# Performance work log

Measured on AMD Instinct MI355X. Metric: run time of the kernel, lower is better.

The kernel has to match this reference:

```python
import jax, jax.numpy as jnp
import numpy as np

T, B, H = 1024, 16, 1024
S = 2048


def setup_inputs() -> dict:
    key = jax.random.key(0)
    k1, k2, k3, k4 = jax.random.split(key, 4)
    output = jax.random.normal(k1, (T, B, H), dtype=jnp.float32)
    memory = jax.random.normal(k2, (S, B, H), dtype=jnp.float32)
    attn_mask = jnp.zeros((B, T, S), dtype=jnp.bool_)  # True = masked
    # linear_out: Linear(2H -> H); torch weight layout [out, in]
    W = jax.random.normal(k3, (H, 2 * H), dtype=jnp.float32) * (1.0 / np.sqrt(2 * H))
    b = jax.random.normal(k4, (H,), dtype=jnp.float32) * 0.01
    return {"output": output, "memory": memory, "attn_mask": attn_mask, "W": W, "b": b}


def reference(output, memory, attn_mask, W, b):
    # scores: (B, T, S) = output^T @ memory (unscaled dot product)
    attn = jnp.einsum('tbh,sbh->bts', output, memory)
    attn = jnp.where(attn_mask, -jnp.inf, attn)
    attn = jax.nn.softmax(attn, axis=2)
    # context: (T, B, H)
    context = jnp.einsum('bts,sbh->tbh', attn, memory)
    combined = jnp.concatenate([context, output], axis=2)  # (T, B, 2H)
    out = jnp.tanh(jnp.einsum('tbd,hd->tbh', combined, W) + b)
    return (out, attn)
```

## Files before the change

### kernel.cpp

```cpp
#include <hip/hip_runtime.h>
#include <hip/hip_bf16.h>
#include <math.h>

#define Tn 1024
#define Bn 16
#define Hn 1024
#define Sn 2048

typedef __attribute__((ext_vector_type(8))) short bf16x8;
typedef __attribute__((ext_vector_type(8))) unsigned short u16x8;
typedef __attribute__((ext_vector_type(4))) float f32x4;

__device__ __forceinline__ unsigned short f2bf(float x) {
  unsigned u = __float_as_uint(x);
  u += 0x7fffu + ((u >> 16) & 1u);
  return (unsigned short)(u >> 16);
}
__device__ __forceinline__ float bf2f(unsigned short h) {
  return __uint_as_float(((unsigned)h) << 16);
}

__device__ __forceinline__ void gload16(const void* g, void* l) {
  __builtin_amdgcn_global_load_lds((const __attribute__((address_space(1))) void*)g,
                                   (__attribute__((address_space(3))) void*)l, 16, 0, 0);
}


__global__ __launch_bounds__(256) void k_split_plane(const float* __restrict__ src,
                                                     unsigned short* __restrict__ hiP,
                                                     unsigned short* __restrict__ loP,
                                                     int rows) {
  const int i = blockIdx.x * 256 + threadIdx.x;
  const int h8 = i & (Hn / 8 - 1);
  const int rem = i >> 7;
  const int b = rem & (Bn - 1);
  const int r = rem >> 4;
  const float4 a = *(const float4*)(src + (size_t)i * 8);
  const float4 c = *(const float4*)(src + (size_t)i * 8 + 4);
  const float v[8] = {a.x, a.y, a.z, a.w, c.x, c.y, c.z, c.w};
  u16x8 hv, lv;
#pragma unroll
  for (int j = 0; j < 8; ++j) {
    const unsigned short h = f2bf(v[j]);
    hv[j] = h;
    lv[j] = f2bf(v[j] - bf2f(h));
  }
  const size_t dst = ((size_t)b * rows + r) * Hn + h8 * 8;
  *(u16x8*)(hiP + dst) = hv;
  *(u16x8*)(loP + dst) = lv;
}

__global__ __launch_bounds__(256) void k_cvt8(const float* __restrict__ src,
                                              unsigned short* __restrict__ dst, int n8) {
  const int i = blockIdx.x * 256 + threadIdx.x;
  if (i >= n8) return;
  const float4 a = *(const float4*)(src + (size_t)i * 8);
  const float4 c = *(const float4*)(src + (size_t)i * 8 + 4);
  u16x8 u;
  u[0] = f2bf(a.x); u[1] = f2bf(a.y); u[2] = f2bf(a.z); u[3] = f2bf(a.w);
  u[4] = f2bf(c.x); u[5] = f2bf(c.y); u[6] = f2bf(c.z); u[7] = f2bf(c.w);
  *(u16x8*)(dst + (size_t)i * 8) = u;
}

__global__ __launch_bounds__(256) void k_trH(const unsigned short* __restrict__ memH,
                                             unsigned short* __restrict__ memT) {
  __shared__ unsigned short L[64 * 72];
  const int t = threadIdx.x;
  const int h0 = blockIdx.x * 64, s0 = blockIdx.y * 64, b = blockIdx.z;
#pragma unroll
  for (int p = 0; p < 2; ++p) {
    const int fid = p * 256 + t;
    const int s_l = fid >> 3;
    const int c = fid & 7;
    const u16x8 v = *(const u16x8*)(memH + ((size_t)b * Sn + s0 + s_l) * Hn + h0 + c * 8);
#pragma unroll
    for (int e = 0; e < 8; ++e) L[(c * 8 + e) * 72 + s_l] = v[e];
  }
  __syncthreads();
#pragma unroll
  for (int p = 0; p < 2; ++p) {
    const int cid = p * 256 + t;
    const int h_l = cid >> 3;
    const int c = cid & 7;
    const u16x8 vv = *(const u16x8*)&L[h_l * 72 + c * 8];
    *(u16x8*)(memT + ((size_t)b * Hn + h0 + h_l) * Sn + s0 + c * 8) = vv;
  }
}


__device__ __forceinline__ void stage128x32(const unsigned short* __restrict__ g, size_t ldr,
                                            unsigned short* __restrict__ lds, int tid) {
  const int wv = tid >> 6;
  const int row = tid >> 2;
  const size_t coff = (size_t)(tid & 3) * 8;
#pragma unroll
  for (int q = 0; q < 2; ++q)
    gload16(g + (size_t)(q * 64 + row) * ldr + coff, lds + q * 2048 + wv * 512);
}

__device__ __forceinline__ void stage128x64(const unsigned short* __restrict__ g, size_t ldr,
                                            unsigned short* __restrict__ lds, int tid) {
  const int wv = tid >> 6;
  const int row = tid >> 3;
  const size_t coff = (size_t)(tid & 7) * 8;
#pragma unroll
  for (int q = 0; q < 4; ++q)
    gload16(g + (size_t)(q * 32 + row) * ldr + coff, lds + q * 2048 + wv * 512);
}


__global__ __launch_bounds__(256, 2) void k_scores(const unsigned short* __restrict__ oH,
                                                   const unsigned short* __restrict__ oL,
                                                   const unsigned short* __restrict__ mH,
                                                   const unsigned short* __restrict__ mL,
                                                   float* __restrict__ attn) {
  __shared__ unsigned short AsH[2][128 * 32], AsL[2][128 * 32];
  __shared__ unsigned short BsH[2][128 * 32], BsL[2][128 * 32];
  const int tid = threadIdx.x, lane = tid & 63, wv = tid >> 6;
  const int wm = (wv >> 1) * 64, wn = (wv & 1) * 64;
  const int bs = blockIdx.x * 128, bt = blockIdx.y * 128, b = blockIdx.z;
  const f32x4 fz = {0.f, 0.f, 0.f, 0.f};
  f32x4 acc[4][4];
#pragma unroll
  for (int i = 0; i < 4; ++i)
#pragma unroll
    for (int j = 0; j < 4; ++j) acc[i][j] = fz;

  const unsigned short* AgH = oH + ((size_t)b * Tn + bt) * Hn;
  const unsigned short* AgL = oL + ((size_t)b * Tn + bt) * Hn;
  const unsigned short* BgH = mH + ((size_t)b * Sn + bs) * Hn;
  const unsigned short* BgL = mL + ((size_t)b * Sn + bs) * Hn;
  const int r16 = lane & 15, kh = (lane >> 4) * 8;
  const int NK = Hn / 32;

  stage128x32(AgH, Hn, AsH[0], tid);
  stage128x32(AgL, Hn, AsL[0], tid);
  stage128x32(BgH, Hn, BsH[0], tid);
  stage128x32(BgL, Hn, BsL[0], tid);
  __syncthreads();

#pragma unroll 2
  for (int t = 0; t < NK; ++t) {
    const int cur = t & 1;
    if (t + 1 < NK) {
      const int k0 = (t + 1) * 32;
      stage128x32(AgH + k0, Hn, AsH[cur ^ 1], tid);
      stage128x32(AgL + k0, Hn, AsL[cur ^ 1], tid);
      stage128x32(BgH + k0, Hn, BsH[cur ^ 1], tid);
      stage128x32(BgL + k0, Hn, BsL[cur ^ 1], tid);
    }
    const unsigned short* AH = AsH[cur];
    const unsigned short* AL = AsL[cur];
    const unsigned short* BH = BsH[cur];
    const unsigned short* BL = BsL[cur];
    bf16x8 ah[4], al[4];
#pragma unroll
    for (int i = 0; i < 4; ++i) {
      ah[i] = *(const bf16x8*)&AH[(wm + i * 16 + r16) * 32 + kh];
      al[i] = *(const bf16x8*)&AL[(wm + i * 16 + r16) * 32 + kh];
    }
#pragma unroll
    for (int j = 0; j < 4; ++j) {
      const bf16x8 bh = *(const bf16x8*)&BH[(wn + j * 16 + r16) * 32 + kh];
      const bf16x8 bl = *(const bf16x8*)&BL[(wn + j * 16 + r16) * 32 + kh];
#pragma unroll
      for (int i = 0; i < 4; ++i) {
        acc[i][j] = __builtin_amdgcn_mfma_f32_16x16x32_bf16(ah[i], bh, acc[i][j], 0, 0, 0);
        acc[i][j] = __builtin_amdgcn_mfma_f32_16x16x32_bf16(ah[i], bl, acc[i][j], 0, 0, 0);
        acc[i][j] = __builtin_amdgcn_mfma_f32_16x16x32_bf16(al[i], bh, acc[i][j], 0, 0, 0);
      }
    }
    __syncthreads();
  }
  const int rq = (lane >> 4) * 4;
  float* obase = attn + (size_t)b * Tn * Sn;
#pragma unroll
  for (int i = 0; i < 4; ++i)
#pragma unroll
    for (int q = 0; q < 4; ++q) {
      const int t = bt + wm + i * 16 + rq + q;
#pragma unroll
      for (int j = 0; j < 4; ++j) {
        const int s = bs + wn + j * 16 + r16;
        obase[(size_t)t * Sn + s] = acc[i][j][q];
      }
    }
}


__global__ __launch_bounds__(256) void k_softmax(float* __restrict__ attn,
                                                 const unsigned char* __restrict__ mask,
                                                 unsigned short* __restrict__ attnbf) {
  const int row = blockIdx.x;
  float* p = attn + (size_t)row * Sn;
  const unsigned char* mrow = mask + (size_t)row * Sn;
  const int tid = threadIdx.x;
  const int lane = tid & 63;
  const int wv = tid >> 6;
  const float4 a = *(const float4*)(p + tid * 8);
  const float4 c = *(const float4*)(p + tid * 8 + 4);
  const unsigned long long mv = *(const unsigned long long*)(mrow + tid * 8);
  float x[8] = {a.x, a.y, a.z, a.w, c.x, c.y, c.z, c.w};
#pragma unroll
  for (int j = 0; j < 8; ++j)
    if ((mv >> (8 * j)) & 0xffull) x[j] = -INFINITY;
  float mx = x[0];
#pragma unroll
  for (int j = 1; j < 8; ++j) mx = fmaxf(mx, x[j]);
#pragma unroll
  for (int off = 32; off; off >>= 1) mx = fmaxf(mx, __shfl_xor(mx, off, 64));
  __shared__ float redmax[4], redsum[4];
  if (lane == 0) redmax[wv] = mx;
  __syncthreads();
  mx = fmaxf(fmaxf(redmax[0], redmax[1]), fmaxf(redmax[2], redmax[3]));
  float e[8];
  float s = 0.f;
#pragma unroll
  for (int j = 0; j < 8; ++j) {
    e[j] = __expf(x[j] - mx);
    s += e[j];
  }
#pragma unroll
  for (int off = 32; off; off >>= 1) s += __shfl_xor(s, off, 64);
  if (lane == 0) redsum[wv] = s;
  __syncthreads();
  s = redsum[0] + redsum[1] + redsum[2] + redsum[3];
  const float inv = 1.0f / s;
  float o[8];
#pragma unroll
  for (int j = 0; j < 8; ++j) o[j] = e[j] * inv;
  float4 o0 = {o[0], o[1], o[2], o[3]};
  float4 o1 = {o[4], o[5], o[6], o[7]};
  *(float4*)(p + tid * 8) = o0;
  *(float4*)(p + tid * 8 + 4) = o1;
  u16x8 ub;
#pragma unroll
  for (int j = 0; j < 8; ++j) ub[j] = f2bf(o[j]);
  *(u16x8*)(attnbf + (size_t)row * Sn + tid * 8) = ub;
}


__device__ __forceinline__ void mfma64(const unsigned short* __restrict__ A,
                                       const unsigned short* __restrict__ B,
                                       int wm, int wn, int lane, f32x4 (&acc)[4][4]) {
  const int r16 = lane & 15;
  const int kh = (lane >> 4) * 8;
#pragma unroll
  for (int ks = 0; ks < 2; ++ks) {
    bf16x8 a[4], bb[4];
#pragma unroll
    for (int i = 0; i < 4; ++i) a[i] = *(const bf16x8*)&A[(wm + i * 16 + r16) * 64 + ks * 32 + kh];
#pragma unroll
    for (int j = 0; j < 4; ++j) bb[j] = *(const bf16x8*)&B[(wn + j * 16 + r16) * 64 + ks * 32 + kh];
#pragma unroll
    for (int i = 0; i < 4; ++i)
#pragma unroll
      for (int j = 0; j < 4; ++j)
        acc[i][j] = __builtin_amdgcn_mfma_f32_16x16x32_bf16(a[i], bb[j], acc[i][j], 0, 0, 0);
  }
}

__global__ __launch_bounds__(256, 2) void k_context(const unsigned short* __restrict__ attnbf,
                                                    const unsigned short* __restrict__ memT,
                                                    unsigned short* __restrict__ ctxB) {
  __shared__ unsigned short As[2][128 * 64], Bs[2][128 * 64];
  const int tid = threadIdx.x, lane = tid & 63, wv = tid >> 6;
  const int wm = (wv >> 1) * 64, wn = (wv & 1) * 64;
  const int bh = blockIdx.x * 128, bt = blockIdx.y * 128, b = blockIdx.z;
  const f32x4 fz = {0.f, 0.f, 0.f, 0.f};
  f32x4 acc[4][4];
#pragma unroll
  for (int i = 0; i < 4; ++i)
#pragma unroll
    for (int j = 0; j < 4; ++j) acc[i][j] = fz;

  const unsigned short* Ag = attnbf + ((size_t)b * Tn + bt) * Sn;
  const unsigned short* Bg = memT + ((size_t)b * Hn + bh) * Sn;
  const int NK = Sn / 64;
  stage128x64(Ag, Sn, As[0], tid);
  stage128x64(Bg, Sn, Bs[0], tid);
  __syncthreads();
#pragma unroll 2
  for (int t = 0; t < NK; ++t) {
    const int cur = t & 1;
    if (t + 1 < NK) {
      const int k0 = (t + 1) * 64;
      stage128x64(Ag + k0, Sn, As[cur ^ 1], tid);
      stage128x64(Bg + k0, Sn, Bs[cur ^ 1], tid);
    }
    mfma64(As[cur], Bs[cur], wm, wn, lane, acc);
    __syncthreads();
  }
  const int r16 = lane & 15, rq = (lane >> 4) * 4;
#pragma unroll
  for (int i = 0; i < 4; ++i)
#pragma unroll
    for (int q = 0; q < 4; ++q) {
      const int t = bt + wm + i * 16 + rq + q;
#pragma unroll
      for (int j = 0; j < 4; ++j) {
        const int h = bh + wn + j * 16 + r16;
        ctxB[((size_t)b * Tn + t) * Hn + h] = f2bf(acc[i][j][q]);
      }
    }
}

__global__ __launch_bounds__(256, 2) void k_final(const unsigned short* __restrict__ ctxB,
                                                  const unsigned short* __restrict__ outpH,
                                                  const unsigned short* __restrict__ Wbf,
                                                  const float* __restrict__ bias,
                                                  float* __restrict__ out) {
  __shared__ unsigned short As[2][128 * 64], Bs[2][128 * 64];
  const int tid = threadIdx.x, lane = tid & 63, wv = tid >> 6;
  const int wm = (wv >> 1) * 64, wn = (wv & 1) * 64;
  const int bh = blockIdx.x * 128, bm = blockIdx.y * 128;
  const f32x4 fz = {0.f, 0.f, 0.f, 0.f};
  f32x4 acc[4][4];
#pragma unroll
  for (int i = 0; i < 4; ++i)
#pragma unroll
    for (int j = 0; j < 4; ++j) acc[i][j] = fz;

  const int NK = (2 * Hn) / 64;
  auto Asrc = [&](int t) -> const unsigned short* {
    const int k0 = t * 64;
    return (k0 < Hn) ? (ctxB + (size_t)bm * Hn + k0) : (outpH + (size_t)bm * Hn + (k0 - Hn));
  };
  stage128x64(Asrc(0), Hn, As[0], tid);
  stage128x64(Wbf + (size_t)bh * (2 * Hn), 2 * Hn, Bs[0], tid);
  __syncthreads();
#pragma unroll 2
  for (int t = 0; t < NK; ++t) {
    const int cur = t & 1;
    if (t + 1 < NK) {
      stage128x64(Asrc(t + 1), Hn, As[cur ^ 1], tid);
      stage128x64(Wbf + (size_t)bh * (2 * Hn) + (t + 1) * 64, 2 * Hn, Bs[cur ^ 1], tid);
    }
    mfma64(As[cur], Bs[cur], wm, wn, lane, acc);
    __syncthreads();
  }
  const int r16 = lane & 15, rq = (lane >> 4) * 4;
  float bj[4];
#pragma unroll
  for (int j = 0; j < 4; ++j) bj[j] = bias[bh + wn + j * 16 + r16];
#pragma unroll
  for (int i = 0; i < 4; ++i)
#pragma unroll
    for (int q = 0; q < 4; ++q) {
      const int r = bm + wm + i * 16 + rq + q;
      const int b = r >> 10, t = r & (Tn - 1);
#pragma unroll
      for (int j = 0; j < 4; ++j) {
        const int h = bh + wn + j * 16 + r16;
        out[((size_t)t * Bn + b) * Hn + h] = tanhf(acc[i][j][q] + bj[j]);
      }
    }
}

extern "C" void kernel_launch(void* const* d_in, const int* in_sizes, int n_in,
                              void* d_out, int out_size, void* d_ws, size_t ws_size,
                              hipStream_t stream) {
  const float* outp = (const float*)d_in[0];
  const float* mem = (const float*)d_in[1];
  const unsigned char* mask = (const unsigned char*)d_in[2];
  const float* W = (const float*)d_in[3];
  const float* bias = (const float*)d_in[4];
  float* out = (float*)d_out;
  float* attn = out + (size_t)Tn * Bn * Hn;

  char* w = (char*)d_ws;
  unsigned short* memH  = (unsigned short*)(w);
  unsigned short* memL  = (unsigned short*)(w + ((size_t)64 << 20));
  unsigned short* outpH = (unsigned short*)(w + ((size_t)128 << 20));
  unsigned short* outpL = (unsigned short*)(w + ((size_t)160 << 20));
  unsigned short* Wbf   = (unsigned short*)(w + ((size_t)192 << 20));
  unsigned short* memT   = memL;
  unsigned short* attnbf = memH;
  unsigned short* ctxB   = outpL;

  k_split_plane<<<dim3((Tn * Bn * Hn / 8) / 256), 256, 0, stream>>>(outp, outpH, outpL, Tn);
  k_split_plane<<<dim3((Sn * Bn * Hn / 8) / 256), 256, 0, stream>>>(mem, memH, memL, Sn);
  k_cvt8<<<dim3((Hn * 2 * Hn / 8) / 256), 256, 0, stream>>>(W, Wbf, Hn * 2 * Hn / 8);

  k_scores<<<dim3(Sn / 128, Tn / 128, Bn), 256, 0, stream>>>(outpH, outpL, memH, memL, attn);
  k_trH<<<dim3(Hn / 64, Sn / 64, Bn), 256, 0, stream>>>(memH, memT);
  k_softmax<<<dim3(Bn * Tn), 256, 0, stream>>>(attn, mask, attnbf);
  k_context<<<dim3(Hn / 128, Tn / 128, Bn), 256, 0, stream>>>(attnbf, memT, ctxB);
  k_final<<<dim3(Hn / 128, (Tn * Bn) / 128), 256, 0, stream>>>(ctxB, outpH, Wbf, bias, out);
}
```

Baseline: 618.1 us.

## Enlarge GEMM tiles to 256x256 with 8 waves, swizzled LDS, finer waits

The three MFMA GEMM kernels (scores, context, final) now use 256x256 block tiles with 512 threads. Each wave computes a 128x64 sub-tile, which raises data reuse per LDS load and halves the number of blocks. LDS staging uses an XOR swizzle to avoid bank conflicts. The full __syncthreads is replaced by explicit vmcnt waits plus s_barrier and s_setprio around the MFMA bursts, to overlap global loads with compute. The costs are larger LDS use (128 KB in scores), more accumulator registers, and fewer blocks, which reduces occupancy and tail balance.

```diff
diff --git a/kernel.cpp b/kernel.cpp
--- a/kernel.cpp
+++ b/kernel.cpp
@@ -88,41 +88,43 @@
 }
 
 
-__device__ __forceinline__ void stage128x32(const unsigned short* __restrict__ g, size_t ldr,
+__device__ __forceinline__ void stage256x64(const unsigned short* __restrict__ g, size_t ldr,
                                             unsigned short* __restrict__ lds, int tid) {
-  const int wv = tid >> 6;
-  const int row = tid >> 2;
-  const size_t coff = (size_t)(tid & 3) * 8;
-#pragma unroll
-  for (int q = 0; q < 2; ++q)
-    gload16(g + (size_t)(q * 64 + row) * ldr + coff, lds + q * 2048 + wv * 512);
-}
-
-__device__ __forceinline__ void stage128x64(const unsigned short* __restrict__ g, size_t ldr,
+#pragma unroll
+  for (int r = 0; r < 4; ++r) {
+    const int row = r * 64 + (tid >> 3);
+    const int cb = (tid & 7) * 16;
+    const int cs = cb ^ ((row & 4) << 3);
+    gload16((const char*)g + (size_t)row * ldr * 2 + cs, (char*)lds + r * 8192 + tid * 16);
+  }
+}
+
+__device__ __forceinline__ void stage256x32(const unsigned short* __restrict__ g, size_t ldr,
                                             unsigned short* __restrict__ lds, int tid) {
-  const int wv = tid >> 6;
-  const int row = tid >> 3;
-  const size_t coff = (size_t)(tid & 7) * 8;
-#pragma unroll
-  for (int q = 0; q < 4; ++q)
-    gload16(g + (size_t)(q * 32 + row) * ldr + coff, lds + q * 2048 + wv * 512);
-}
-
-
-__global__ __launch_bounds__(256, 2) void k_scores(const unsigned short* __restrict__ oH,
+#pragma unroll
+  for (int r = 0; r < 2; ++r) {
+    const int row = r * 128 + (tid >> 2);
+    const int cb = (tid & 3) * 16;
+    const int cs = cb ^ ((row & 8) << 2);
+    gload16((const char*)g + (size_t)row * ldr * 2 + cs, (char*)lds + r * 8192 + tid * 16);
+  }
+}
+
+
+__global__ __launch_bounds__(512, 2) void k_scores(const unsigned short* __restrict__ oH,
                                                    const unsigned short* __restrict__ oL,
                                                    const unsigned short* __restrict__ mH,
                                                    const unsigned short* __restrict__ mL,
                                                    float* __restrict__ attn) {
-  __shared__ unsigned short AsH[2][128 * 32], AsL[2][128 * 32];
-  __shared__ unsigned short BsH[2][128 * 32], BsL[2][128 * 32];
+  __shared__ unsigned short AsH[2][256 * 32], AsL[2][256 * 32];
+  __shared__ unsigned short BsH[2][256 * 32], BsL[2][256 * 32];
   const int tid = threadIdx.x, lane = tid & 63, wv = tid >> 6;
-  const int wm = (wv >> 1) * 64, wn = (wv & 1) * 64;
-  const int bs = blockIdx.x * 128, bt = blockIdx.y * 128, b = blockIdx.z;
+  const int wr = wv >> 2, wc = wv & 3;
+  const int bs = blockIdx.x * 256, bt = blockIdx.y * 256, b = blockIdx.z;
   const f32x4 fz = {0.f, 0.f, 0.f, 0.f};
-  f32x4 acc[4][4];
-#pragma unroll
-  for (int i = 0; i < 4; ++i)
+  f32x4 acc[8][4];
+#pragma unroll
+  for (int i = 0; i < 8; ++i)
 #pragma unroll
     for (int j = 0; j < 4; ++j) acc[i][j] = fz;
 
@@ -130,61 +132,83 @@
   const unsigned short* AgL = oL + ((size_t)b * Tn + bt) * Hn;
   const unsigned short* BgH = mH + ((size_t)b * Sn + bs) * Hn;
   const unsigned short* BgL = mL + ((size_t)b * Sn + bs) * Hn;
-  const int r16 = lane & 15, kh = (lane >> 4) * 8;
+  const int r16 = lane & 15, khB = (lane >> 4) * 16;
   const int NK = Hn / 32;
 
-  stage128x32(AgH, Hn, AsH[0], tid);
-  stage128x32(AgL, Hn, AsL[0], tid);
-  stage128x32(BgH, Hn, BsH[0], tid);
-  stage128x32(BgL, Hn, BsL[0], tid);
-  __syncthreads();
-
-#pragma unroll 2
+  stage256x32(AgH, Hn, AsH[0], tid);
+  stage256x32(AgL, Hn, AsL[0], tid);
+  stage256x32(BgH, Hn, BsH[0], tid);
+  stage256x32(BgL, Hn, BsL[0], tid);
+
   for (int t = 0; t < NK; ++t) {
     const int cur = t & 1;
     if (t + 1 < NK) {
       const int k0 = (t + 1) * 32;
-      stage128x32(AgH + k0, Hn, AsH[cur ^ 1], tid);
-      stage128x32(AgL + k0, Hn, AsL[cur ^ 1], tid);
-      stage128x32(BgH + k0, Hn, BsH[cur ^ 1], tid);
-      stage128x32(BgL + k0, Hn, BsL[cur ^ 1], tid);
-    }
-    const unsigned short* AH = AsH[cur];
-    const unsigned short* AL = AsL[cur];
-    const unsigned short* BH = BsH[cur];
-    const unsigned short* BL = BsL[cur];
-    bf16x8 ah[4], al[4];
-#pragma unroll
-    for (int i = 0; i < 4; ++i) {
-      ah[i] = *(const bf16x8*)&AH[(wm + i * 16 + r16) * 32 + kh];
-      al[i] = *(const bf16x8*)&AL[(wm + i * 16 + r16) * 32 + kh];
-    }
-#pragma unroll
-    for (int j = 0; j < 4; ++j) {
-      const bf16x8 bh = *(const bf16x8*)&BH[(wn + j * 16 + r16) * 32 + kh];
-      const bf16x8 bl = *(const bf16x8*)&BL[(wn + j * 16 + r16) * 32 + kh];
-#pragma unroll
-      for (int i = 0; i < 4; ++i) {
-        acc[i][j] = __builtin_amdgcn_mfma_f32_16x16x32_bf16(ah[i], bh, acc[i][j], 0, 0, 0);
-        acc[i][j] = __builtin_amdgcn_mfma_f32_16x16x32_bf16(ah[i], bl, acc[i][j], 0, 0, 0);
-        acc[i][j] = __builtin_amdgcn_mfma_f32_16x16x32_bf16(al[i], bh, acc[i][j], 0, 0, 0);
-      }
-    }
-    __syncthreads();
+      stage256x32(AgH + k0, Hn, AsH[cur ^ 1], tid);
+      stage256x32(AgL + k0, Hn, AsL[cur ^ 1], tid);
+      stage256x32(BgH + k0, Hn, BsH[cur ^ 1], tid);
+      stage256x32(BgL + k0, Hn, BsL[cur ^ 1], tid);
+      asm volatile("s_waitcnt vmcnt(8)" ::: "memory");
+    } else {
+      asm volatile("s_waitcnt vmcnt(0)" ::: "memory");
+    }
+    __builtin_amdgcn_s_barrier();
+
+    const char* ABh = (const char*)AsH[cur];
+    const char* ABl = (const char*)AsL[cur];
+    const char* BBh = (const char*)BsH[cur];
+    const char* BBl = (const char*)BsL[cur];
+    bf16x8 bh[2][2], bl[2][2];
+#pragma unroll
+    for (int nq = 0; nq < 2; ++nq)
+#pragma unroll
+      for (int fj = 0; fj < 2; ++fj) {
+        const int rb = wc * 64 + nq * 32 + fj * 16 + r16;
+        const int off = rb * 64 + (khB ^ ((rb & 8) << 2));
+        bh[nq][fj] = *(const bf16x8*)(BBh + off);
+        bl[nq][fj] = *(const bf16x8*)(BBl + off);
+      }
+#pragma unroll
+    for (int mq = 0; mq < 2; ++mq) {
+      bf16x8 ah[4], al[4];
+#pragma unroll
+      for (int fi = 0; fi < 4; ++fi) {
+        const int ra = wr * 128 + mq * 64 + fi * 16 + r16;
+        const int off = ra * 64 + (khB ^ ((ra & 8) << 2));
+        ah[fi] = *(const bf16x8*)(ABh + off);
+        al[fi] = *(const bf16x8*)(ABl + off);
+      }
+      __builtin_amdgcn_s_setprio(1);
+#pragma unroll
+      for (int nq = 0; nq < 2; ++nq)
+#pragma unroll
+        for (int fj = 0; fj < 2; ++fj)
+#pragma unroll
+          for (int fi = 0; fi < 4; ++fi) {
+            f32x4& a = acc[mq * 4 + fi][nq * 2 + fj];
+            a = __builtin_amdgcn_mfma_f32_16x16x32_bf16(ah[fi], bh[nq][fj], a, 0, 0, 0);
+            a = __builtin_amdgcn_mfma_f32_16x16x32_bf16(ah[fi], bl[nq][fj], a, 0, 0, 0);
+            a = __builtin_amdgcn_mfma_f32_16x16x32_bf16(al[fi], bh[nq][fj], a, 0, 0, 0);
+          }
+      __builtin_amdgcn_s_setprio(0);
+    }
+    __builtin_amdgcn_s_barrier();
   }
   const int rq = (lane >> 4) * 4;
   float* obase = attn + (size_t)b * Tn * Sn;
 #pragma unroll
-  for (int i = 0; i < 4; ++i)
+  for (int i = 0; i < 8; ++i) {
+    const int m_off = wr * 128 + (i >> 2) * 64 + (i & 3) * 16;
 #pragma unroll
     for (int q = 0; q < 4; ++q) {
-      const int t = bt + wm + i * 16 + rq + q;
+      const int t = bt + m_off + rq + q;
 #pragma unroll
       for (int j = 0; j < 4; ++j) {
-        const int s = bs + wn + j * 16 + r16;
+        const int s = bs + wc * 64 + (j >> 1) * 32 + (j & 1) * 16 + r16;
         obase[(size_t)t * Sn + s] = acc[i][j][q];
       }
     }
+  }
 }
 
 
@@ -240,121 +264,194 @@
 }
 
 
-__device__ __forceinline__ void mfma64(const unsigned short* __restrict__ A,
-                                       const unsigned short* __restrict__ B,
-                                       int wm, int wn, int lane, f32x4 (&acc)[4][4]) {
-  const int r16 = lane & 15;
-  const int kh = (lane >> 4) * 8;
-#pragma unroll
-  for (int ks = 0; ks < 2; ++ks) {
-    bf16x8 a[4], bb[4];
-#pragma unroll
-    for (int i = 0; i < 4; ++i) a[i] = *(const bf16x8*)&A[(wm + i * 16 + r16) * 64 + ks * 32 + kh];
-#pragma unroll
-    for (int j = 0; j < 4; ++j) bb[j] = *(const bf16x8*)&B[(wn + j * 16 + r16) * 64 + ks * 32 + kh];
-#pragma unroll
-    for (int i = 0; i < 4; ++i)
-#pragma unroll
-      for (int j = 0; j < 4; ++j)
-        acc[i][j] = __builtin_amdgcn_mfma_f32_16x16x32_bf16(a[i], bb[j], acc[i][j], 0, 0, 0);
-  }
-}
-
-__global__ __launch_bounds__(256, 2) void k_context(const unsigned short* __restrict__ attnbf,
+__global__ __launch_bounds__(512, 2) void k_context(const unsigned short* __restrict__ attnbf,
                                                     const unsigned short* __restrict__ memT,
                                                     unsigned short* __restrict__ ctxB) {
-  __shared__ unsigned short As[2][128 * 64], Bs[2][128 * 64];
+  __shared__ unsigned short As[2][256 * 64], Bs[2][256 * 64];
   const int tid = threadIdx.x, lane = tid & 63, wv = tid >> 6;
-  const int wm = (wv >> 1) * 64, wn = (wv & 1) * 64;
-  const int bh = blockIdx.x * 128, bt = blockIdx.y * 128, b = blockIdx.z;
+  const int wr = wv >> 2, wc = wv & 3;
+  const int bh = blockIdx.x * 256, bt = blockIdx.y * 256, b = blockIdx.z;
   const f32x4 fz = {0.f, 0.f, 0.f, 0.f};
-  f32x4 acc[4][4];
-#pragma unroll
-  for (int i = 0; i < 4; ++i)
+  f32x4 acc[8][4];
+#pragma unroll
+  for (int i = 0; i < 8; ++i)
 #pragma unroll
     for (int j = 0; j < 4; ++j) acc[i][j] = fz;
 
   const unsigned short* Ag = attnbf + ((size_t)b * Tn + bt) * Sn;
   const unsigned short* Bg = memT + ((size_t)b * Hn + bh) * Sn;
+  const int r16 = lane & 15, khB = (lane >> 4) * 16;
   const int NK = Sn / 64;
-  stage128x64(Ag, Sn, As[0], tid);
-  stage128x64(Bg, Sn, Bs[0], tid);
-  __syncthreads();
-#pragma unroll 2
+
+  stage256x64(Ag, Sn, As[0], tid);
+  stage256x64(Bg, Sn, Bs[0], tid);
+
   for (int t = 0; t < NK; ++t) {
     const int cur = t & 1;
     if (t + 1 < NK) {
       const int k0 = (t + 1) * 64;
-      stage128x64(Ag + k0, Sn, As[cur ^ 1], tid);
-      stage128x64(Bg + k0, Sn, Bs[cur ^ 1], tid);
-    }
-    mfma64(As[cur], Bs[cur], wm, wn, lane, acc);
-    __syncthreads();
-  }
-  const int r16 = lane & 15, rq = (lane >> 4) * 4;
-#pragma unroll
-  for (int i = 0; i < 4; ++i)
+      stage256x64(Ag + k0, Sn, As[cur ^ 1], tid);
+      stage256x64(Bg + k0, Sn, Bs[cur ^ 1], tid);
+      asm volatile("s_waitcnt vmcnt(8)" ::: "memory");
+    } else {
+      asm volatile("s_waitcnt vmcnt(0)" ::: "memory");
+    }
+    __builtin_amdgcn_s_barrier();
+
+    const char* Ab = (const char*)As[cur];
+    const char* Bb = (const char*)Bs[cur];
+    bf16x8 bb[2][2][2];
+#pragma unroll
+    for (int nq = 0; nq < 2; ++nq)
+#pragma unroll
+      for (int fj = 0; fj < 2; ++fj) {
+        const int rb = wc * 64 + nq * 32 + fj * 16 + r16;
+#pragma unroll
+        for (int ks = 0; ks < 2; ++ks) {
+          const int cb = ks * 64 + khB;
+          bb[nq][fj][ks] = *(const bf16x8*)(Bb + rb * 128 + (cb ^ ((rb & 4) << 3)));
+        }
+      }
+#pragma unroll
+    for (int mq = 0; mq < 2; ++mq) {
+      bf16x8 aa[4][2];
+#pragma unroll
+      for (int fi = 0; fi < 4; ++fi) {
+        const int ra = wr * 128 + mq * 64 + fi * 16 + r16;
+#pragma unroll
+        for (int ks = 0; ks < 2; ++ks) {
+          const int cb = ks * 64 + khB;
+          aa[fi][ks] = *(const bf16x8*)(Ab + ra * 128 + (cb ^ ((ra & 4) << 3)));
+        }
+      }
+      __builtin_amdgcn_s_setprio(1);
+#pragma unroll
+      for (int nq = 0; nq < 2; ++nq)
+#pragma unroll
+        for (int fj = 0; fj < 2; ++fj)
+#pragma unroll
+          for (int fi = 0; fi < 4; ++fi)
+#pragma unroll
+            for (int ks = 0; ks < 2; ++ks) {
+              f32x4& a = acc[mq * 4 + fi][nq * 2 + fj];
+              a = __builtin_amdgcn_mfma_f32_16x16x32_bf16(aa[fi][ks], bb[nq][fj][ks], a, 0, 0, 0);
+            }
+      __builtin_amdgcn_s_setprio(0);
+    }
+    __builtin_amdgcn_s_barrier();
+  }
+  const int rq = (lane >> 4) * 4;
+#pragma unroll
+  for (int i = 0; i < 8; ++i) {
+    const int m_off = wr * 128 + (i >> 2) * 64 + (i & 3) * 16;
 #pragma unroll
     for (int q = 0; q < 4; ++q) {
-      const int t = bt + wm + i * 16 + rq + q;
+      const int t = bt + m_off + rq + q;
 #pragma unroll
       for (int j = 0; j < 4; ++j) {
-        const int h = bh + wn + j * 16 + r16;
+        const int h = bh + wc * 64 + (j >> 1) * 32 + (j & 1) * 16 + r16;
         ctxB[((size_t)b * Tn + t) * Hn + h] = f2bf(acc[i][j][q]);
       }
     }
-}
-
-__global__ __launch_bounds__(256, 2) void k_final(const unsigned short* __restrict__ ctxB,
+  }
+}
+
+
+__global__ __launch_bounds__(512, 2) void k_final(const unsigned short* __restrict__ ctxB,
                                                   const unsigned short* __restrict__ outpH,
                                                   const unsigned short* __restrict__ Wbf,
                                                   const float* __restrict__ bias,
                                                   float* __restrict__ out) {
-  __shared__ unsigned short As[2][128 * 64], Bs[2][128 * 64];
+  __shared__ unsigned short As[2][256 * 64], Bs[2][256 * 64];
   const int tid = threadIdx.x, lane = tid & 63, wv = tid >> 6;
-  const int wm = (wv >> 1) * 64, wn = (wv & 1) * 64;
-  const int bh = blockIdx.x * 128, bm = blockIdx.y * 128;
+  const int wr = wv >> 2, wc = wv & 3;
+  const int bh = blockIdx.x * 256, bm = blockIdx.y * 256;
   const f32x4 fz = {0.f, 0.f, 0.f, 0.f};
-  f32x4 acc[4][4];
-#pragma unroll
-  for (int i = 0; i < 4; ++i)
+  f32x4 acc[8][4];
+#pragma unroll
+  for (int i = 0; i < 8; ++i)
 #pragma unroll
     for (int j = 0; j < 4; ++j) acc[i][j] = fz;
 
+  const int r16 = lane & 15, khB = (lane >> 4) * 16;
   const int NK = (2 * Hn) / 64;
-  auto Asrc = [&](int t) -> const unsigned short* {
-    const int k0 = t * 64;
-    return (k0 < Hn) ? (ctxB + (size_t)bm * Hn + k0) : (outpH + (size_t)bm * Hn + (k0 - Hn));
+  auto Asrc = [&](int tt) -> const unsigned short* {
+    return (tt < 16) ? (ctxB + (size_t)bm * Hn + tt * 64)
+                     : (outpH + (size_t)bm * Hn + (tt - 16) * 64);
   };
-  stage128x64(Asrc(0), Hn, As[0], tid);
-  stage128x64(Wbf + (size_t)bh * (2 * Hn), 2 * Hn, Bs[0], tid);
-  __syncthreads();
-#pragma unroll 2
+  const unsigned short* Bg = Wbf + (size_t)bh * (2 * Hn);
+
+  stage256x64(Asrc(0), Hn, As[0], tid);
+  stage256x64(Bg, 2 * Hn, Bs[0], tid);
+
   for (int t = 0; t < NK; ++t) {
     const int cur = t & 1;
     if (t + 1 < NK) {
-      stage128x64(Asrc(t + 1), Hn, As[cur ^ 1], tid);
-      stage128x64(Wbf + (size_t)bh * (2 * Hn) + (t + 1) * 64, 2 * Hn, Bs[cur ^ 1], tid);
-    }
-    mfma64(As[cur], Bs[cur], wm, wn, lane, acc);
-    __syncthreads();
-  }
-  const int r16 = lane & 15, rq = (lane >> 4) * 4;
-  float bj[4];
-#pragma unroll
-  for (int j = 0; j < 4; ++j) bj[j] = bias[bh + wn + j * 16 + r16];
-#pragma unroll
-  for (int i = 0; i < 4; ++i)
+      stage256x64(Asrc(t + 1), Hn, As[cur ^ 1], tid);
+      stage256x64(Bg + (t + 1) * 64, 2 * Hn, Bs[cur ^ 1], tid);
+      asm volatile("s_waitcnt vmcnt(8)" ::: "memory");
+    } else {
+      asm volatile("s_waitcnt vmcnt(0)" ::: "memory");
+    }
+    __builtin_amdgcn_s_barrier();
+
+    const char* Ab = (const char*)As[cur];
+    const char* Bb = (const char*)Bs[cur];
+    bf16x8 bb[2][2][2];
+#pragma unroll
+    for (int nq = 0; nq < 2; ++nq)
+#pragma unroll
+      for (int fj = 0; fj < 2; ++fj) {
+        const int rb = wc * 64 + nq * 32 + fj * 16 + r16;
+#pragma unroll
+        for (int ks = 0; ks < 2; ++ks) {
+          const int cb = ks * 64 + khB;
+          bb[nq][fj][ks] = *(const bf16x8*)(Bb + rb * 128 + (cb ^ ((rb & 4) << 3)));
+        }
+      }
+#pragma unroll
+    for (int mq = 0; mq < 2; ++mq) {
+      bf16x8 aa[4][2];
+#pragma unroll
+      for (int fi = 0; fi < 4; ++fi) {
+        const int ra = wr * 128 + mq * 64 + fi * 16 + r16;
+#pragma unroll
+        for (int ks = 0; ks < 2; ++ks) {
+          const int cb = ks * 64 + khB;
+          aa[fi][ks] = *(const bf16x8*)(Ab + ra * 128 + (cb ^ ((ra & 4) << 3)));
+        }
+      }
+      __builtin_amdgcn_s_setprio(1);
+#pragma unroll
+      for (int nq = 0; nq < 2; ++nq)
+#pragma unroll
+        for (int fj = 0; fj < 2; ++fj)
+#pragma unroll
+          for (int fi = 0; fi < 4; ++fi)
+#pragma unroll
+            for (int ks = 0; ks < 2; ++ks) {
+              f32x4& a = acc[mq * 4 + fi][nq * 2 + fj];
+              a = __builtin_amdgcn_mfma_f32_16x16x32_bf16(aa[fi][ks], bb[nq][fj][ks], a, 0, 0, 0);
+            }
+      __builtin_amdgcn_s_setprio(0);
+    }
+    __builtin_amdgcn_s_barrier();
+  }
+  const int rq = (lane >> 4) * 4;
+#pragma unroll
+  for (int i = 0; i < 8; ++i) {
+    const int m_off = wr * 128 + (i >> 2) * 64 + (i & 3) * 16;
 #pragma unroll
     for (int q = 0; q < 4; ++q) {
-      const int r = bm + wm + i * 16 + rq + q;
+      const int r = bm + m_off + rq + q;
       const int b = r >> 10, t = r & (Tn - 1);
 #pragma unroll
       for (int j = 0; j < 4; ++j) {
-        const int h = bh + wn + j * 16 + r16;
-        out[((size_t)t * Bn + b) * Hn + h] = tanhf(acc[i][j][q] + bj[j]);
-      }
-    }
+        const int h = bh + wc * 64 + (j >> 1) * 32 + (j & 1) * 16 + r16;
+        out[((size_t)t * Bn + b) * Hn + h] = tanhf(acc[i][j][q] + bias[h]);
+      }
+    }
+  }
 }
 
 extern "C" void kernel_launch(void* const* d_in, const int* in_sizes, int n_in,
@@ -382,9 +479,9 @@
   k_split_plane<<<dim3((Sn * Bn * Hn / 8) / 256), 256, 0, stream>>>(mem, memH, memL, Sn);
   k_cvt8<<<dim3((Hn * 2 * Hn / 8) / 256), 256, 0, stream>>>(W, Wbf, Hn * 2 * Hn / 8);
 
-  k_scores<<<dim3(Sn / 128, Tn / 128, Bn), 256, 0, stream>>>(outpH, outpL, memH, memL, attn);
+  k_scores<<<dim3(Sn / 256, Tn / 256, Bn), 512, 0, stream>>>(outpH, outpL, memH, memL, attn);
   k_trH<<<dim3(Hn / 64, Sn / 64, Bn), 256, 0, stream>>>(memH, memT);
   k_softmax<<<dim3(Bn * Tn), 256, 0, stream>>>(attn, mask, attnbf);
-  k_context<<<dim3(Hn / 128, Tn / 128, Bn), 256, 0, stream>>>(attnbf, memT, ctxB);
-  k_final<<<dim3(Hn / 128, (Tn * Bn) / 128), 256, 0, stream>>>(ctxB, outpH, Wbf, bias, out);
-}
+  k_context<<<dim3(Hn / 256, Tn / 256, Bn), 512, 0, stream>>>(attnbf, memT, ctxB);
+  k_final<<<dim3(Hn / 256, (Tn * Bn) / 256), 512, 0, stream>>>(ctxB, outpH, Wbf, bias, out);
+}
```

Measured after the change: 550.6 us. 10.9% less time.
